# Kernel tuning notes

Measured on AMD Instinct MI355X. Metric: run time of the kernel, lower is better.

The kernel has to match this reference:

```python
import jax, jax.numpy as jnp
import numpy as np

DIM = 1280
NUM_HEADS = 16
HEAD_DIM = DIM // NUM_HEADS  # 80
SEQ = 3072


def rotate_half(x):
    half = x.shape[-1] // 2
    return jnp.concatenate([-x[..., half:], x[..., :half]], axis=-1)


def apply_rotary_pos_emb_vision(t, freqs):
    # t: [seq, heads, head_dim]; freqs: [seq, head_dim//2]
    emb = jnp.concatenate([freqs, freqs], axis=-1)  # [seq, head_dim]
    cos = jnp.cos(emb)[:, None, :]
    sin = jnp.sin(emb)[:, None, :]
    return t * cos + rotate_half(t) * sin


def setup_inputs() -> dict:
    key = jax.random.key(0)
    k1, k2, k3, k4, k5 = jax.random.split(key, 5)
    hidden_states = jax.random.normal(k1, (SEQ, DIM), dtype=jnp.float32)
    rotary_pos_emb = jax.random.uniform(k2, (SEQ, HEAD_DIM // 2), dtype=jnp.float32) * 10.0
    cu_seqlens = jnp.arange(5, dtype=jnp.int32) * (SEQ // 4)  # [0,768,1536,2304,3072]
    s = 1.0 / np.sqrt(DIM)
    qkv_w = jax.random.normal(k3, (3 * DIM, DIM), dtype=jnp.float32) * s
    qkv_b = jnp.zeros((3 * DIM,), dtype=jnp.float32)
    proj_w = jax.random.normal(k4, (DIM, DIM), dtype=jnp.float32) * s
    proj_b = jnp.zeros((DIM,), dtype=jnp.float32)
    return {
        "hidden_states": hidden_states,
        "rotary_pos_emb": rotary_pos_emb,
        "cu_seqlens": cu_seqlens,
        "qkv_w": qkv_w,
        "qkv_b": qkv_b,
        "proj_w": proj_w,
        "proj_b": proj_b,
    }


def reference(hidden_states, rotary_pos_emb, cu_seqlens, qkv_w, qkv_b, proj_w, proj_b):
    seq = hidden_states.shape[0]
    qkv = hidden_states @ qkv_w.T + qkv_b  # [seq, 3*dim]
    qkv = qkv.reshape(seq, 3, NUM_HEADS, HEAD_DIM)
    q, k, v = qkv[:, 0], qkv[:, 1], qkv[:, 2]  # each [seq, heads, head_dim]

    q = apply_rotary_pos_emb_vision(q, rotary_pos_emb)
    k = apply_rotary_pos_emb_vision(k, rotary_pos_emb)

    # block-diagonal mask from cu_seqlens: tokens attend only within own segment
    pos = jnp.arange(seq)
    seg = jnp.searchsorted(cu_seqlens[1:], pos, side="right")  # segment id per token
    mask = seg[:, None] == seg[None, :]  # [seq, seq] bool

    # [heads, seq, head_dim]
    qh = q.transpose(1, 0, 2)
    kh = k.transpose(1, 0, 2)
    vh = v.transpose(1, 0, 2)

    scale = 1.0 / np.sqrt(HEAD_DIM)
    scores = jnp.einsum("hqd,hkd->hqk", qh, kh) * scale
    scores = jnp.where(mask[None], scores, jnp.finfo(scores.dtype).min)
    attn = jax.nn.softmax(scores, axis=-1)
    out = jnp.einsum("hqk,hkd->hqd", attn, vh)  # [heads, seq, head_dim]

    out = out.transpose(1, 0, 2).reshape(seq, DIM)
    return out @ proj_w.T + proj_b
```

## Files before the change

### kernel.cpp

```cpp
#include <hip/hip_runtime.h>
#include <cstdint>
#include <cstddef>

#define SEQ 3072
#define DIM 1280
#define NH 16
#define HD 80

typedef __attribute__((ext_vector_type(8))) short s16x8;
typedef __attribute__((ext_vector_type(4))) float f32x4;
typedef unsigned short u16;
typedef unsigned int u32;
typedef unsigned long long u64;

__device__ __forceinline__ u16 f2bf(float f) {
  u32 u = __builtin_bit_cast(u32, f);
  u32 r = (u + 0x7FFFu + ((u >> 16) & 1u)) >> 16;
  return (u16)r;
}
__device__ __forceinline__ float bf2f(u16 b) {
  u32 u = ((u32)b) << 16;
  return __builtin_bit_cast(float, u);
}
__device__ __forceinline__ u32 cvtpk_bf16(float lo, float hi) {
  u32 r;
  asm("v_cvt_pk_bf16_f32 %0, %1, %2" : "=v"(r) : "v"(lo), "v"(hi));
  return r;
}
__device__ __forceinline__ void gload16(const u16* g, u16* lds) {
  __builtin_amdgcn_global_load_lds((const __attribute__((address_space(1))) void*)g,
                                   (__attribute__((address_space(3))) void*)lds,
                                   16, 0, 0);
}

#define N4_A (SEQ*DIM/4)
#define N4_B (3*DIM*DIM/4)
#define N4_C (DIM*DIM/4)
__global__ void cvt_kernel(const float* __restrict__ sa, u16* __restrict__ da,
                           const float* __restrict__ sb, u16* __restrict__ db,
                           const float* __restrict__ sc, u16* __restrict__ dc) {
  int i = blockIdx.x * blockDim.x + threadIdx.x;
  const float* s; u16* d; int j;
  if (i < N4_A)            { s = sa; d = da; j = i; }
  else if (i < N4_A+N4_B)  { s = sb; d = db; j = i - N4_A; }
  else if (i < N4_A+N4_B+N4_C) { s = sc; d = dc; j = i - N4_A - N4_B; }
  else return;
  float4 v = ((const float4*)s)[j];
  ushort4 o;
  o.x = f2bf(v.x); o.y = f2bf(v.y); o.z = f2bf(v.z); o.w = f2bf(v.w);
  ((ushort4*)d)[j] = o;
}

template<int MODE>
__global__ __launch_bounds__(256)
void gemm_kernel(const u16* __restrict__ A, const u16* __restrict__ B,
                 const float* __restrict__ bias,
                 u16* __restrict__ qws, u16* __restrict__ kws, u16* __restrict__ vT,
                 float* __restrict__ fout,
                 int M, int N, int K)
{
  constexpr int BM = 128, BN = 128, BK = 32;
  __shared__ __align__(16) u16 As[2][BM*BK];
  __shared__ __align__(16) u16 Bs[2][BN*BK];
  const int m0 = blockIdx.y * BM, n0 = blockIdx.x * BN;
  const int tid = threadIdx.x;
  const int lane = tid & 63, wave = tid >> 6;
  const int wr = wave >> 1, wc = wave & 1;
  const int lr = lane & 15, lg = lane >> 4;

  const int c0 = tid, c1 = 256 + tid;
  const int r0 = c0 >> 2, cc0 = c0 & 3;
  const int r1 = c1 >> 2, cc1 = c1 & 3;
  const int wb0 = (tid & ~63), wb1 = 256 + (tid & ~63);

  f32x4 acc[4][4];
  #pragma unroll
  for (int i = 0; i < 4; ++i)
    #pragma unroll
    for (int j = 0; j < 4; ++j) acc[i][j] = (f32x4)0.0f;

  const int NT = K / BK;

  gload16(A + (size_t)(m0 + r0)*K + cc0*8, &As[0][0] + wb0*8);
  gload16(B + (size_t)(n0 + r0)*K + cc0*8, &Bs[0][0] + wb0*8);
  gload16(A + (size_t)(m0 + r1)*K + cc1*8, &As[0][0] + wb1*8);
  gload16(B + (size_t)(n0 + r1)*K + cc1*8, &Bs[0][0] + wb1*8);
  __syncthreads();

  int cur = 0;
  for (int t = 0; t < NT; ++t) {
    if (t + 1 < NT) {
      const int k0 = (t + 1) * BK;
      const int nxt = cur ^ 1;
      gload16(A + (size_t)(m0 + r0)*K + k0 + cc0*8, &As[nxt][0] + wb0*8);
      gload16(B + (size_t)(n0 + r0)*K + k0 + cc0*8, &Bs[nxt][0] + wb0*8);
      gload16(A + (size_t)(m0 + r1)*K + k0 + cc1*8, &As[nxt][0] + wb1*8);
      gload16(B + (size_t)(n0 + r1)*K + k0 + cc1*8, &Bs[nxt][0] + wb1*8);
    }
    s16x8 af[4], bf[4];
    #pragma unroll
    for (int i = 0; i < 4; ++i) {
      af[i] = *(const s16x8*)&As[cur][(wr*64 + i*16 + lr)*BK + lg*8];
      bf[i] = *(const s16x8*)&Bs[cur][(wc*64 + i*16 + lr)*BK + lg*8];
    }
    #pragma unroll
    for (int mi = 0; mi < 4; ++mi)
      #pragma unroll
      for (int ni = 0; ni < 4; ++ni)
        acc[mi][ni] = __builtin_amdgcn_mfma_f32_16x16x32_bf16(af[mi], bf[ni], acc[mi][ni], 0, 0, 0);
    __syncthreads();
    cur ^= 1;
  }

  #pragma unroll
  for (int ni = 0; ni < 4; ++ni) {
    const int n = n0 + wc*64 + ni*16 + lr;
    const float bv = bias[n];
    if constexpr (MODE == 0) {
      const int which = n / DIM;
      const int hd = n - which*DIM;
      const int h = hd / HD;
      const int d = hd - h*HD;
      #pragma unroll
      for (int mi = 0; mi < 4; ++mi) {
        const int mb = m0 + wr*64 + mi*16 + lg*4;
        #pragma unroll
        for (int j = 0; j < 4; ++j) {
          const u16 b = f2bf(acc[mi][ni][j] + bv);
          const int m = mb + j;
          if (which == 0)      qws[((size_t)h*SEQ + m)*HD + d] = b;
          else if (which == 1) kws[((size_t)h*SEQ + m)*HD + d] = b;
          else                 vT [((size_t)h*HD + d)*SEQ + m] = b;
        }
      }
    } else {
      #pragma unroll
      for (int mi = 0; mi < 4; ++mi) {
        const int mb = m0 + wr*64 + mi*16 + lg*4;
        #pragma unroll
        for (int j = 0; j < 4; ++j)
          fout[(size_t)(mb + j)*N + n] = acc[mi][ni][j] + bv;
      }
    }
  }
}

__global__ void rope_tab_kernel(const float* __restrict__ freqs, float2* __restrict__ tab, int n) {
  int i = blockIdx.x*blockDim.x + threadIdx.x;
  if (i >= n) return;
  float f = freqs[i];
  tab[i] = make_float2(cosf(f), sinf(f));
}

__global__ void rope_apply_kernel(u16* __restrict__ q, u16* __restrict__ k,
                                  const float2* __restrict__ tab) {
  int idx = blockIdx.x*blockDim.x + threadIdx.x;
  if (idx >= NH*SEQ*5) return;
  const int c = idx % 5;
  const int s = (idx / 5) % SEQ;
  const int h = idx / (5*SEQ);
  const int d0 = c*8;
  const float2* tp = tab + s*(HD/2) + d0;
  float cs[8], sn[8];
  #pragma unroll
  for (int j = 0; j < 8; ++j) { float2 f = tp[j]; cs[j] = f.x; sn[j] = f.y; }
  const size_t base = ((size_t)h*SEQ + s)*HD;
  {
    s16x8 x = *(const s16x8*)(q + base + d0);
    s16x8 y = *(const s16x8*)(q + base + (HD/2) + d0);
    s16x8 nx, ny;
    #pragma unroll
    for (int j = 0; j < 8; ++j) {
      float xv = bf2f((u16)x[j]), yv = bf2f((u16)y[j]);
      nx[j] = (short)f2bf(xv*cs[j] - yv*sn[j]);
      ny[j] = (short)f2bf(yv*cs[j] + xv*sn[j]);
    }
    *(s16x8*)(q + base + d0) = nx;
    *(s16x8*)(q + base + (HD/2) + d0) = ny;
  }
  {
    s16x8 x = *(const s16x8*)(k + base + d0);
    s16x8 y = *(const s16x8*)(k + base + (HD/2) + d0);
    s16x8 nx, ny;
    #pragma unroll
    for (int j = 0; j < 8; ++j) {
      float xv = bf2f((u16)x[j]), yv = bf2f((u16)y[j]);
      nx[j] = (short)f2bf(xv*cs[j] - yv*sn[j]);
      ny[j] = (short)f2bf(yv*cs[j] + xv*sn[j]);
    }
    *(s16x8*)(k + base + d0) = nx;
    *(s16x8*)(k + base + (HD/2) + d0) = ny;
  }
}


struct AttnState {
  float m_run[2];
  float lp[2];
  f32x4 oacc[2][5];
};

__device__ __forceinline__ void load_kv(const u16* __restrict__ kbase,
                                        const u16* __restrict__ vbase,
                                        int lr, int lg, int kc,
                                        s16x8 (&KF)[2][3], s16x8 (&VF)[5]) {
  int kcl = kc; if (kcl > SEQ-32) kcl = SEQ-32;
  #pragma unroll
  for (int kt = 0; kt < 2; ++kt)
    #pragma unroll
    for (int s = 0; s < 3; ++s) {
      const int d0 = s*32 + lg*8;
      if (d0 < HD) KF[kt][s] = *(const s16x8*)(kbase + (size_t)(kcl + kt*16 + lr)*HD + d0);
      else         KF[kt][s] = (s16x8)(short)0;
    }
  #pragma unroll
  for (int dt = 0; dt < 5; ++dt)
    VF[dt] = *(const s16x8*)(vbase + (size_t)(dt*16 + lr)*SEQ + kcl + lg*8);
}

__device__ __forceinline__ void compute_chunk(int kc, const s16x8 (&KF)[2][3], const s16x8 (&VF)[5],
                                              const s16x8 (&qf)[2][3], AttnState& st,
                                              u16 (&P_lds)[2][16][32],
                                              int lr, int lg, int swz,
                                              int rs0, int re0, int rs1, int re1) {
  const float NEG = -__builtin_inff();
  const float DTH = 8.0f;
  const float kscale = 0.11180339887498949f * 1.44269504088896341f;

  f32x4 sacc[2][2];
  #pragma unroll
  for (int qs = 0; qs < 2; ++qs)
    #pragma unroll
    for (int kt = 0; kt < 2; ++kt) sacc[qs][kt] = (f32x4)0.0f;
  #pragma unroll
  for (int kt = 0; kt < 2; ++kt)
    #pragma unroll
    for (int s = 0; s < 3; ++s) {
      sacc[0][kt] = __builtin_amdgcn_mfma_f32_16x16x32_bf16(KF[kt][s], qf[0][s], sacc[0][kt], 0, 0, 0);
      sacc[1][kt] = __builtin_amdgcn_mfma_f32_16x16x32_bf16(KF[kt][s], qf[1][s], sacc[1][kt], 0, 0, 0);
    }

  float sv[2][8];
  #pragma unroll
  for (int qs = 0; qs < 2; ++qs)
    #pragma unroll
    for (int kt = 0; kt < 2; ++kt)
      #pragma unroll
      for (int j = 0; j < 4; ++j)
        sv[qs][kt*4+j] = sacc[qs][kt][j] * kscale;

  const bool full = __all((kc >= rs0) && (kc+32 <= re0) && (kc >= rs1) && (kc+32 <= re1));
  if (!full) {
    #pragma unroll
    for (int qs = 0; qs < 2; ++qs) {
      const int rsq = qs ? rs1 : rs0, req = qs ? re1 : re0;
      #pragma unroll
      for (int kt = 0; kt < 2; ++kt)
        #pragma unroll
        for (int j = 0; j < 4; ++j) {
          const int key = kc + kt*16 + lg*4 + j;
          if (key < rsq || key >= req) sv[qs][kt*4+j] = NEG;
        }
    }
  }

  float pc[2];
  #pragma unroll
  for (int qs = 0; qs < 2; ++qs) {
    float c = sv[qs][0];
    #pragma unroll
    for (int i = 1; i < 8; ++i) c = fmaxf(c, sv[qs][i]);
    pc[qs] = c;
  }

  const bool nore = __all((pc[0] - st.m_run[0] <= DTH) && (pc[1] - st.m_run[1] <= DTH));
  u32 pk[2][4];
  if (nore) {
    #pragma unroll
    for (int qs = 0; qs < 2; ++qs) {
      const float m = st.m_run[qs];
      float ps = 0.0f;
      #pragma unroll
      for (int i2 = 0; i2 < 4; ++i2) {
        float pa = __builtin_amdgcn_exp2f(sv[qs][2*i2]   - m);
        float pb = __builtin_amdgcn_exp2f(sv[qs][2*i2+1] - m);
        ps += pa + pb;
        pk[qs][i2] = cvtpk_bf16(pa, pb);
      }
      st.lp[qs] += ps;
    }
  } else {
    #pragma unroll
    for (int qs = 0; qs < 2; ++qs) {
      float c = pc[qs];
      c = fmaxf(c, __shfl_xor(c, 16, 64));
      c = fmaxf(c, __shfl_xor(c, 32, 64));
      const float mn = fmaxf(st.m_run[qs], c);
      const float fs = (mn == st.m_run[qs]) ? 1.0f : __builtin_amdgcn_exp2f(st.m_run[qs] - mn);
      float ps = 0.0f;
      #pragma unroll
      for (int i2 = 0; i2 < 4; ++i2) {
        float a0 = sv[qs][2*i2], a1 = sv[qs][2*i2+1];
        float pa = (a0 == NEG) ? 0.0f : __builtin_amdgcn_exp2f(a0 - mn);
        float pb = (a1 == NEG) ? 0.0f : __builtin_amdgcn_exp2f(a1 - mn);
        ps += pa + pb;
        pk[qs][i2] = cvtpk_bf16(pa, pb);
      }
      st.lp[qs] = st.lp[qs] * fs + ps;
      st.m_run[qs] = mn;
      float fr[4];
      #pragma unroll
      for (int j = 0; j < 4; ++j)
        fr[j] = __builtin_bit_cast(float,
                  __builtin_amdgcn_ds_bpermute((lg*4 + j)*4, __builtin_bit_cast(int, fs)));
      #pragma unroll
      for (int dt = 0; dt < 5; ++dt)
        #pragma unroll
        for (int j = 0; j < 4; ++j) st.oacc[qs][dt][j] *= fr[j];
    }
  }

  #pragma unroll
  for (int qs = 0; qs < 2; ++qs) {
    u64 w0 = (u64)pk[qs][0] | ((u64)pk[qs][1] << 32);
    u64 w1 = (u64)pk[qs][2] | ((u64)pk[qs][3] << 32);
    u64* P64 = (u64*)&P_lds[qs][0][0];
    P64[lr*8 + ( lg      ^ (swz<<1))] = w0;
    P64[lr*8 + ((4 + lg) ^ (swz<<1))] = w1;
  }
  s16x8 pa0 = *(const s16x8*)&P_lds[0][lr][(lg ^ swz) * 8];
  s16x8 pa1 = *(const s16x8*)&P_lds[1][lr][(lg ^ swz) * 8];

  #pragma unroll
  for (int dt = 0; dt < 5; ++dt) {
    st.oacc[0][dt] = __builtin_amdgcn_mfma_f32_16x16x32_bf16(pa0, VF[dt], st.oacc[0][dt], 0, 0, 0);
    st.oacc[1][dt] = __builtin_amdgcn_mfma_f32_16x16x32_bf16(pa1, VF[dt], st.oacc[1][dt], 0, 0, 0);
  }
}

__global__ __launch_bounds__(64)
void attn_kernel(const u16* __restrict__ qws, const u16* __restrict__ kws,
                 const u16* __restrict__ vT, const int* __restrict__ cu, int ncu,
                 u16* __restrict__ ows )
{
  __shared__ __align__(16) u16 P_lds[2][16][32];
  const int h = blockIdx.x & 15;
  const int t = blockIdx.x >> 4;
  const int lane = threadIdx.x;
  const int lr = lane & 15, lg = lane >> 4;
  const int q0 = t*32;
  const float NEG = -__builtin_inff();

  int rs0 = cu[0], re0 = cu[1], rs1 = cu[0], re1 = cu[1];
  int ts = cu[0], te = cu[1];
  {
    const int qa = q0 + lr, qb = q0 + 16 + lr;
    for (int i = 1; i < ncu-1; ++i) {
      int lo = cu[i], hi = cu[i+1];
      if (qa    >= lo) { rs0 = lo; re0 = hi; }
      if (qb    >= lo) { rs1 = lo; re1 = hi; }
      if (q0    >= lo) { ts = lo; }
      if (q0+31 >= lo) { te = hi; }
    }
  }

  const u16* kbase = kws + (size_t)h*SEQ*HD;
  const u16* vbase = vT  + (size_t)h*HD*SEQ;

  s16x8 qf[2][3];
  #pragma unroll
  for (int qs = 0; qs < 2; ++qs)
    #pragma unroll
    for (int s = 0; s < 3; ++s) {
      int d0 = s*32 + lg*8;
      if (d0 < HD) qf[qs][s] = *(const s16x8*)(qws + ((size_t)h*SEQ + q0 + qs*16 + lr)*HD + d0);
      else         qf[qs][s] = (s16x8)(short)0;
    }

  AttnState st;
  st.m_run[0] = NEG; st.m_run[1] = NEG;
  st.lp[0] = 0.0f;   st.lp[1] = 0.0f;
  #pragma unroll
  for (int qs = 0; qs < 2; ++qs)
    #pragma unroll
    for (int dt = 0; dt < 5; ++dt) st.oacc[qs][dt] = (f32x4)0.0f;

  const int swz = (lr >> 1) & 3;

  const int kc0 = ts & ~31;
  const int nch = (te - kc0 + 31) >> 5;

  s16x8 kfA[2][3], vfA[5], kfB[2][3], vfB[5];
  load_kv(kbase, vbase, lr, lg, kc0, kfA, vfA);

  int kc = kc0, i = 0;
  for (; i + 2 <= nch; i += 2) {
    load_kv(kbase, vbase, lr, lg, kc+32, kfB, vfB);
    compute_chunk(kc, kfA, vfA, qf, st, P_lds, lr, lg, swz, rs0, re0, rs1, re1);
    load_kv(kbase, vbase, lr, lg, kc+64, kfA, vfA);
    compute_chunk(kc+32, kfB, vfB, qf, st, P_lds, lr, lg, swz, rs0, re0, rs1, re1);
    kc += 64;
  }
  if (i < nch)
    compute_chunk(kc, kfA, vfA, qf, st, P_lds, lr, lg, swz, rs0, re0, rs1, re1);

  #pragma unroll
  for (int qs = 0; qs < 2; ++qs) {
    float l = st.lp[qs];
    l += __shfl_xor(l, 16, 64);
    l += __shfl_xor(l, 32, 64);
    float linv[4];
    #pragma unroll
    for (int j = 0; j < 4; ++j) {
      float lv = __builtin_bit_cast(float,
                   __builtin_amdgcn_ds_bpermute((lg*4 + j)*4, __builtin_bit_cast(int, l)));
      linv[j] = 1.0f / lv;
    }
    #pragma unroll
    for (int dt = 0; dt < 5; ++dt)
      #pragma unroll
      for (int j = 0; j < 4; ++j) {
        float v = st.oacc[qs][dt][j] * linv[j];
        ows[(size_t)(q0 + qs*16 + lg*4 + j)*DIM + h*HD + dt*16 + lr] = f2bf(v);
      }
  }
}

extern "C" void kernel_launch(void* const* d_in, const int* in_sizes, int n_in,
                              void* d_out, int out_size, void* d_ws, size_t ws_size,
                              hipStream_t stream) {
  const float* hidden = (const float*)d_in[0];
  const float* rope   = (const float*)d_in[1];
  const int*   cu     = (const int*)d_in[2];
  const float* qkv_w  = (const float*)d_in[3];
  const float* qkv_b  = (const float*)d_in[4];
  const float* proj_w = (const float*)d_in[5];
  const float* proj_b = (const float*)d_in[6];
  float* out = (float*)d_out;
  const int ncu = in_sizes[2];

  char* ws = (char*)d_ws;
  u16* Abf = (u16*)ws; ws += (size_t)SEQ*DIM*2;
  u16* Wq  = (u16*)ws; ws += (size_t)3*DIM*DIM*2;
  u16* Wp  = (u16*)ws; ws += (size_t)DIM*DIM*2;
  u16* qws = (u16*)ws; ws += (size_t)NH*SEQ*HD*2;
  u16* kws = (u16*)ws; ws += (size_t)NH*SEQ*HD*2;
  u16* vTw = (u16*)ws; ws += (size_t)NH*SEQ*HD*2;
  u16* ows = (u16*)ws; ws += (size_t)SEQ*DIM*2;

  cvt_kernel<<<(N4_A+N4_B+N4_C+255)/256, 256, 0, stream>>>(hidden, Abf, qkv_w, Wq, proj_w, Wp);

  gemm_kernel<0><<<dim3(3*DIM/128, SEQ/128), 256, 0, stream>>>(
      Abf, Wq, qkv_b, qws, kws, vTw, nullptr, SEQ, 3*DIM, DIM);

  float2* tab = (float2*)Abf;
  rope_tab_kernel<<<(SEQ*(HD/2) + 255)/256, 256, 0, stream>>>(rope, tab, SEQ*(HD/2));
  rope_apply_kernel<<<(NH*SEQ*5 + 255)/256, 256, 0, stream>>>(qws, kws, tab);

  attn_kernel<<<NH*(SEQ/32), 64, 0, stream>>>(qws, kws, vTw, cu, ncu, ows);

  gemm_kernel<1><<<dim3(DIM/128, SEQ/128), 256, 0, stream>>>(
      ows, Wp, proj_b, nullptr, nullptr, nullptr, out, SEQ, DIM, DIM);
}
```

Measured before the change: 156.4 us.

## Triple-buffer GEMM loads with vmcnt waits and shrink attention blocks to 16 queries

The GEMM now prefetches two K-tiles ahead and uses explicit vmcnt/lgkmcnt waits with raw barriers in place of __syncthreads, so global loads can overlap more MFMA work. The attention kernel processes 16 queries per wavefront instead of 32, doubling the grid to raise occupancy and parallelism. It also adds a third K/V register buffer for a deeper software pipeline. The trade-off is that each K/V chunk is loaded for half as many queries, doubling K/V load traffic, and the hand-written waitcnt logic depends on how the compiler orders loads.

```diff
diff --git a/kernel.cpp b/kernel.cpp
--- a/kernel.cpp
+++ b/kernel.cpp
@@ -73,6 +73,14 @@
   const int r1 = c1 >> 2, cc1 = c1 & 3;
   const int wb0 = (tid & ~63), wb1 = 256 + (tid & ~63);
 
+  auto stage = [&](int t, int buf) {
+    const int k0 = t * BK;
+    gload16(A + (size_t)(m0 + r0)*K + k0 + cc0*8, &As[buf][0] + wb0*8);
+    gload16(B + (size_t)(n0 + r0)*K + k0 + cc0*8, &Bs[buf][0] + wb0*8);
+    gload16(A + (size_t)(m0 + r1)*K + k0 + cc1*8, &As[buf][0] + wb1*8);
+    gload16(B + (size_t)(n0 + r1)*K + k0 + cc1*8, &Bs[buf][0] + wb1*8);
+  };
+
   f32x4 acc[4][4];
   #pragma unroll
   for (int i = 0; i < 4; ++i)
@@ -81,22 +89,16 @@
 
   const int NT = K / BK;
 
-  gload16(A + (size_t)(m0 + r0)*K + cc0*8, &As[0][0] + wb0*8);
-  gload16(B + (size_t)(n0 + r0)*K + cc0*8, &Bs[0][0] + wb0*8);
-  gload16(A + (size_t)(m0 + r1)*K + cc1*8, &As[0][0] + wb1*8);
-  gload16(B + (size_t)(n0 + r1)*K + cc1*8, &Bs[0][0] + wb1*8);
-  __syncthreads();
+  stage(0, 0);
+  stage(1, 1);
 
   int cur = 0;
   for (int t = 0; t < NT; ++t) {
-    if (t + 1 < NT) {
-      const int k0 = (t + 1) * BK;
-      const int nxt = cur ^ 1;
-      gload16(A + (size_t)(m0 + r0)*K + k0 + cc0*8, &As[nxt][0] + wb0*8);
-      gload16(B + (size_t)(n0 + r0)*K + k0 + cc0*8, &Bs[nxt][0] + wb0*8);
-      gload16(A + (size_t)(m0 + r1)*K + k0 + cc1*8, &As[nxt][0] + wb1*8);
-      gload16(B + (size_t)(n0 + r1)*K + k0 + cc1*8, &Bs[nxt][0] + wb1*8);
-    }
+    if (t == NT - 1) asm volatile("s_waitcnt vmcnt(0)" ::: "memory");
+    else             asm volatile("s_waitcnt vmcnt(4)" ::: "memory");
+    __builtin_amdgcn_s_barrier();
+    __builtin_amdgcn_sched_barrier(0);
+
     s16x8 af[4], bf[4];
     #pragma unroll
     for (int i = 0; i < 4; ++i) {
@@ -108,7 +110,12 @@
       #pragma unroll
       for (int ni = 0; ni < 4; ++ni)
         acc[mi][ni] = __builtin_amdgcn_mfma_f32_16x16x32_bf16(af[mi], bf[ni], acc[mi][ni], 0, 0, 0);
-    __syncthreads();
+
+    asm volatile("s_waitcnt lgkmcnt(0)" ::: "memory");
+    __builtin_amdgcn_sched_barrier(0);
+    __builtin_amdgcn_s_barrier();
+
+    if (t + 2 < NT) stage(t + 2, cur);
     cur ^= 1;
   }
 
@@ -195,9 +202,9 @@
 
 
 struct AttnState {
-  float m_run[2];
-  float lp[2];
-  f32x4 oacc[2][5];
+  float m_run;
+  float lp;
+  f32x4 oacc[5];
 };
 
 __device__ __forceinline__ void load_kv(const u16* __restrict__ kbase,
@@ -219,123 +226,98 @@
 }
 
 __device__ __forceinline__ void compute_chunk(int kc, const s16x8 (&KF)[2][3], const s16x8 (&VF)[5],
-                                              const s16x8 (&qf)[2][3], AttnState& st,
-                                              u16 (&P_lds)[2][16][32],
+                                              const s16x8 (&qf)[3], AttnState& st,
+                                              u16 (&P_lds)[16][32],
                                               int lr, int lg, int swz,
-                                              int rs0, int re0, int rs1, int re1) {
+                                              int rs0, int re0) {
   const float NEG = -__builtin_inff();
   const float DTH = 8.0f;
   const float kscale = 0.11180339887498949f * 1.44269504088896341f;
 
-  f32x4 sacc[2][2];
-  #pragma unroll
-  for (int qs = 0; qs < 2; ++qs)
-    #pragma unroll
-    for (int kt = 0; kt < 2; ++kt) sacc[qs][kt] = (f32x4)0.0f;
+  f32x4 sacc[2];
+  #pragma unroll
+  for (int kt = 0; kt < 2; ++kt) sacc[kt] = (f32x4)0.0f;
   #pragma unroll
   for (int kt = 0; kt < 2; ++kt)
     #pragma unroll
-    for (int s = 0; s < 3; ++s) {
-      sacc[0][kt] = __builtin_amdgcn_mfma_f32_16x16x32_bf16(KF[kt][s], qf[0][s], sacc[0][kt], 0, 0, 0);
-      sacc[1][kt] = __builtin_amdgcn_mfma_f32_16x16x32_bf16(KF[kt][s], qf[1][s], sacc[1][kt], 0, 0, 0);
-    }
-
-  float sv[2][8];
-  #pragma unroll
-  for (int qs = 0; qs < 2; ++qs)
+    for (int s = 0; s < 3; ++s)
+      sacc[kt] = __builtin_amdgcn_mfma_f32_16x16x32_bf16(KF[kt][s], qf[s], sacc[kt], 0, 0, 0);
+
+  float sv[8];
+  #pragma unroll
+  for (int kt = 0; kt < 2; ++kt)
+    #pragma unroll
+    for (int j = 0; j < 4; ++j)
+      sv[kt*4+j] = sacc[kt][j] * kscale;
+
+  const bool full = __all((kc >= rs0) && (kc+32 <= re0));
+  if (!full) {
     #pragma unroll
     for (int kt = 0; kt < 2; ++kt)
       #pragma unroll
-      for (int j = 0; j < 4; ++j)
-        sv[qs][kt*4+j] = sacc[qs][kt][j] * kscale;
-
-  const bool full = __all((kc >= rs0) && (kc+32 <= re0) && (kc >= rs1) && (kc+32 <= re1));
-  if (!full) {
-    #pragma unroll
-    for (int qs = 0; qs < 2; ++qs) {
-      const int rsq = qs ? rs1 : rs0, req = qs ? re1 : re0;
-      #pragma unroll
-      for (int kt = 0; kt < 2; ++kt)
-        #pragma unroll
-        for (int j = 0; j < 4; ++j) {
-          const int key = kc + kt*16 + lg*4 + j;
-          if (key < rsq || key >= req) sv[qs][kt*4+j] = NEG;
-        }
-    }
-  }
-
-  float pc[2];
-  #pragma unroll
-  for (int qs = 0; qs < 2; ++qs) {
-    float c = sv[qs][0];
-    #pragma unroll
-    for (int i = 1; i < 8; ++i) c = fmaxf(c, sv[qs][i]);
-    pc[qs] = c;
-  }
-
-  const bool nore = __all((pc[0] - st.m_run[0] <= DTH) && (pc[1] - st.m_run[1] <= DTH));
-  u32 pk[2][4];
+      for (int j = 0; j < 4; ++j) {
+        const int key = kc + kt*16 + lg*4 + j;
+        if (key < rs0 || key >= re0) sv[kt*4+j] = NEG;
+      }
+  }
+
+  float pc = sv[0];
+  #pragma unroll
+  for (int i = 1; i < 8; ++i) pc = fmaxf(pc, sv[i]);
+
+  const bool nore = __all(pc - st.m_run <= DTH);
+  u32 pk[4];
   if (nore) {
-    #pragma unroll
-    for (int qs = 0; qs < 2; ++qs) {
-      const float m = st.m_run[qs];
-      float ps = 0.0f;
-      #pragma unroll
-      for (int i2 = 0; i2 < 4; ++i2) {
-        float pa = __builtin_amdgcn_exp2f(sv[qs][2*i2]   - m);
-        float pb = __builtin_amdgcn_exp2f(sv[qs][2*i2+1] - m);
-        ps += pa + pb;
-        pk[qs][i2] = cvtpk_bf16(pa, pb);
-      }
-      st.lp[qs] += ps;
-    }
+    const float m = st.m_run;
+    float ps = 0.0f;
+    #pragma unroll
+    for (int i2 = 0; i2 < 4; ++i2) {
+      float pa = __builtin_amdgcn_exp2f(sv[2*i2]   - m);
+      float pb = __builtin_amdgcn_exp2f(sv[2*i2+1] - m);
+      ps += pa + pb;
+      pk[i2] = cvtpk_bf16(pa, pb);
+    }
+    st.lp += ps;
   } else {
-    #pragma unroll
-    for (int qs = 0; qs < 2; ++qs) {
-      float c = pc[qs];
-      c = fmaxf(c, __shfl_xor(c, 16, 64));
-      c = fmaxf(c, __shfl_xor(c, 32, 64));
-      const float mn = fmaxf(st.m_run[qs], c);
-      const float fs = (mn == st.m_run[qs]) ? 1.0f : __builtin_amdgcn_exp2f(st.m_run[qs] - mn);
-      float ps = 0.0f;
-      #pragma unroll
-      for (int i2 = 0; i2 < 4; ++i2) {
-        float a0 = sv[qs][2*i2], a1 = sv[qs][2*i2+1];
-        float pa = (a0 == NEG) ? 0.0f : __builtin_amdgcn_exp2f(a0 - mn);
-        float pb = (a1 == NEG) ? 0.0f : __builtin_amdgcn_exp2f(a1 - mn);
-        ps += pa + pb;
-        pk[qs][i2] = cvtpk_bf16(pa, pb);
-      }
-      st.lp[qs] = st.lp[qs] * fs + ps;
-      st.m_run[qs] = mn;
-      float fr[4];
-      #pragma unroll
-      for (int j = 0; j < 4; ++j)
-        fr[j] = __builtin_bit_cast(float,
-                  __builtin_amdgcn_ds_bpermute((lg*4 + j)*4, __builtin_bit_cast(int, fs)));
-      #pragma unroll
-      for (int dt = 0; dt < 5; ++dt)
-        #pragma unroll
-        for (int j = 0; j < 4; ++j) st.oacc[qs][dt][j] *= fr[j];
-    }
-  }
-
-  #pragma unroll
-  for (int qs = 0; qs < 2; ++qs) {
-    u64 w0 = (u64)pk[qs][0] | ((u64)pk[qs][1] << 32);
-    u64 w1 = (u64)pk[qs][2] | ((u64)pk[qs][3] << 32);
-    u64* P64 = (u64*)&P_lds[qs][0][0];
+    float c = pc;
+    c = fmaxf(c, __shfl_xor(c, 16, 64));
+    c = fmaxf(c, __shfl_xor(c, 32, 64));
+    const float mn = fmaxf(st.m_run, c);
+    const float fs = (mn == st.m_run) ? 1.0f : __builtin_amdgcn_exp2f(st.m_run - mn);
+    float ps = 0.0f;
+    #pragma unroll
+    for (int i2 = 0; i2 < 4; ++i2) {
+      float a0 = sv[2*i2], a1 = sv[2*i2+1];
+      float pa = (a0 == NEG) ? 0.0f : __builtin_amdgcn_exp2f(a0 - mn);
+      float pb = (a1 == NEG) ? 0.0f : __builtin_amdgcn_exp2f(a1 - mn);
+      ps += pa + pb;
+      pk[i2] = cvtpk_bf16(pa, pb);
+    }
+    st.lp = st.lp * fs + ps;
+    st.m_run = mn;
+    float fr[4];
+    #pragma unroll
+    for (int j = 0; j < 4; ++j)
+      fr[j] = __builtin_bit_cast(float,
+                __builtin_amdgcn_ds_bpermute((lg*4 + j)*4, __builtin_bit_cast(int, fs)));
+    #pragma unroll
+    for (int dt = 0; dt < 5; ++dt)
+      #pragma unroll
+      for (int j = 0; j < 4; ++j) st.oacc[dt][j] *= fr[j];
+  }
+
+  {
+    u64 w0 = (u64)pk[0] | ((u64)pk[1] << 32);
+    u64 w1 = (u64)pk[2] | ((u64)pk[3] << 32);
+    u64* P64 = (u64*)&P_lds[0][0];
     P64[lr*8 + ( lg      ^ (swz<<1))] = w0;
     P64[lr*8 + ((4 + lg) ^ (swz<<1))] = w1;
   }
-  s16x8 pa0 = *(const s16x8*)&P_lds[0][lr][(lg ^ swz) * 8];
-  s16x8 pa1 = *(const s16x8*)&P_lds[1][lr][(lg ^ swz) * 8];
-
-  #pragma unroll
-  for (int dt = 0; dt < 5; ++dt) {
-    st.oacc[0][dt] = __builtin_amdgcn_mfma_f32_16x16x32_bf16(pa0, VF[dt], st.oacc[0][dt], 0, 0, 0);
-    st.oacc[1][dt] = __builtin_amdgcn_mfma_f32_16x16x32_bf16(pa1, VF[dt], st.oacc[1][dt], 0, 0, 0);
-  }
+  s16x8 pa = *(const s16x8*)&P_lds[lr][(lg ^ swz) * 8];
+
+  #pragma unroll
+  for (int dt = 0; dt < 5; ++dt)
+    st.oacc[dt] = __builtin_amdgcn_mfma_f32_16x16x32_bf16(pa, VF[dt], st.oacc[dt], 0, 0, 0);
 }
 
 __global__ __launch_bounds__(64)
@@ -343,70 +325,68 @@
                  const u16* __restrict__ vT, const int* __restrict__ cu, int ncu,
                  u16* __restrict__ ows )
 {
-  __shared__ __align__(16) u16 P_lds[2][16][32];
+  __shared__ __align__(16) u16 P_lds[16][32];
   const int h = blockIdx.x & 15;
   const int t = blockIdx.x >> 4;
   const int lane = threadIdx.x;
   const int lr = lane & 15, lg = lane >> 4;
-  const int q0 = t*32;
+  const int q0 = t*16;
   const float NEG = -__builtin_inff();
 
-  int rs0 = cu[0], re0 = cu[1], rs1 = cu[0], re1 = cu[1];
+  int rs0 = cu[0], re0 = cu[1];
   int ts = cu[0], te = cu[1];
   {
-    const int qa = q0 + lr, qb = q0 + 16 + lr;
+    const int qa = q0 + lr;
     for (int i = 1; i < ncu-1; ++i) {
       int lo = cu[i], hi = cu[i+1];
       if (qa    >= lo) { rs0 = lo; re0 = hi; }
-      if (qb    >= lo) { rs1 = lo; re1 = hi; }
       if (q0    >= lo) { ts = lo; }
-      if (q0+31 >= lo) { te = hi; }
+      if (q0+15 >= lo) { te = hi; }
     }
   }
 
   const u16* kbase = kws + (size_t)h*SEQ*HD;
   const u16* vbase = vT  + (size_t)h*HD*SEQ;
 
-  s16x8 qf[2][3];
-  #pragma unroll
-  for (int qs = 0; qs < 2; ++qs)
-    #pragma unroll
-    for (int s = 0; s < 3; ++s) {
-      int d0 = s*32 + lg*8;
-      if (d0 < HD) qf[qs][s] = *(const s16x8*)(qws + ((size_t)h*SEQ + q0 + qs*16 + lr)*HD + d0);
-      else         qf[qs][s] = (s16x8)(short)0;
-    }
+  s16x8 qf[3];
+  #pragma unroll
+  for (int s = 0; s < 3; ++s) {
+    int d0 = s*32 + lg*8;
+    if (d0 < HD) qf[s] = *(const s16x8*)(qws + ((size_t)h*SEQ + q0 + lr)*HD + d0);
+    else         qf[s] = (s16x8)(short)0;
+  }
 
   AttnState st;
-  st.m_run[0] = NEG; st.m_run[1] = NEG;
-  st.lp[0] = 0.0f;   st.lp[1] = 0.0f;
-  #pragma unroll
-  for (int qs = 0; qs < 2; ++qs)
-    #pragma unroll
-    for (int dt = 0; dt < 5; ++dt) st.oacc[qs][dt] = (f32x4)0.0f;
+  st.m_run = NEG;
+  st.lp = 0.0f;
+  #pragma unroll
+  for (int dt = 0; dt < 5; ++dt) st.oacc[dt] = (f32x4)0.0f;
 
   const int swz = (lr >> 1) & 3;
 
   const int kc0 = ts & ~31;
   const int nch = (te - kc0 + 31) >> 5;
 
-  s16x8 kfA[2][3], vfA[5], kfB[2][3], vfB[5];
-  load_kv(kbase, vbase, lr, lg, kc0, kfA, vfA);
+  s16x8 kfA[2][3], vfA[5], kfB[2][3], vfB[5], kfC[2][3], vfC[5];
+  load_kv(kbase, vbase, lr, lg, kc0,      kfA, vfA);
+  load_kv(kbase, vbase, lr, lg, kc0 + 32, kfB, vfB);
 
   int kc = kc0, i = 0;
-  for (; i + 2 <= nch; i += 2) {
-    load_kv(kbase, vbase, lr, lg, kc+32, kfB, vfB);
-    compute_chunk(kc, kfA, vfA, qf, st, P_lds, lr, lg, swz, rs0, re0, rs1, re1);
-    load_kv(kbase, vbase, lr, lg, kc+64, kfA, vfA);
-    compute_chunk(kc+32, kfB, vfB, qf, st, P_lds, lr, lg, swz, rs0, re0, rs1, re1);
-    kc += 64;
-  }
-  if (i < nch)
-    compute_chunk(kc, kfA, vfA, qf, st, P_lds, lr, lg, swz, rs0, re0, rs1, re1);
-
-  #pragma unroll
-  for (int qs = 0; qs < 2; ++qs) {
-    float l = st.lp[qs];
+  for (; i + 3 <= nch; i += 3) {
+    load_kv(kbase, vbase, lr, lg, kc+64,  kfC, vfC);
+    compute_chunk(kc,    kfA, vfA, qf, st, P_lds, lr, lg, swz, rs0, re0);
+    load_kv(kbase, vbase, lr, lg, kc+96,  kfA, vfA);
+    compute_chunk(kc+32, kfB, vfB, qf, st, P_lds, lr, lg, swz, rs0, re0);
+    load_kv(kbase, vbase, lr, lg, kc+128, kfB, vfB);
+    compute_chunk(kc+64, kfC, vfC, qf, st, P_lds, lr, lg, swz, rs0, re0);
+    kc += 96;
+  }
+  const int rem = nch - i;
+  if (rem >= 1) compute_chunk(kc,    kfA, vfA, qf, st, P_lds, lr, lg, swz, rs0, re0);
+  if (rem == 2) compute_chunk(kc+32, kfB, vfB, qf, st, P_lds, lr, lg, swz, rs0, re0);
+
+  {
+    float l = st.lp;
     l += __shfl_xor(l, 16, 64);
     l += __shfl_xor(l, 32, 64);
     float linv[4];
@@ -420,8 +400,8 @@
     for (int dt = 0; dt < 5; ++dt)
       #pragma unroll
       for (int j = 0; j < 4; ++j) {
-        float v = st.oacc[qs][dt][j] * linv[j];
-        ows[(size_t)(q0 + qs*16 + lg*4 + j)*DIM + h*HD + dt*16 + lr] = f2bf(v);
+        float v = st.oacc[dt][j] * linv[j];
+        ows[(size_t)(q0 + lg*4 + j)*DIM + h*HD + dt*16 + lr] = f2bf(v);
       }
   }
 }
@@ -457,7 +437,7 @@
   rope_tab_kernel<<<(SEQ*(HD/2) + 255)/256, 256, 0, stream>>>(rope, tab, SEQ*(HD/2));
   rope_apply_kernel<<<(NH*SEQ*5 + 255)/256, 256, 0, stream>>>(qws, kws, tab);
 
-  attn_kernel<<<NH*(SEQ/32), 64, 0, stream>>>(qws, kws, vTw, cu, ncu, ows);
+  attn_kernel<<<NH*(SEQ/16), 64, 0, stream>>>(qws, kws, vTw, cu, ncu, ows);
 
   gemm_kernel<1><<<dim3(DIM/128, SEQ/128), 256, 0, stream>>>(
       ows, Wp, proj_b, nullptr, nullptr, nullptr, out, SEQ, DIM, DIM);
```

Measured after the change: 168.5 us. 7.7% more time.

## Share K/V tiles across two waves via double-buffered LDS staging in attention

Applied to the files above, without the earlier changes.

The attention kernel now launches 128-thread blocks covering 64 query rows. K and V chunks of 64 keys are loaded cooperatively into double-buffered shared memory with direct global-to-LDS loads, and both waves read their MFMA operands from there. Each K/V tile is fetched from global memory once per two waves instead of once per wave, and the key chunk grows from 32 to 64. The costs are a __syncthreads per chunk, more LDS per block, and more registers for the larger score tile, which may lower occupancy. Segment bounds are now computed over the 64-row block, so waves near segment edges can scan more masked keys.

```diff
diff --git a/kernel.cpp b/kernel.cpp
--- a/kernel.cpp
+++ b/kernel.cpp
@@ -6,6 +6,8 @@
 #define DIM 1280
 #define NH 16
 #define HD 80
+#define QB 64
+#define KB 64
 
 typedef __attribute__((ext_vector_type(8))) short s16x8;
 typedef __attribute__((ext_vector_type(4))) float f32x4;
@@ -193,179 +195,63 @@
   }
 }
 
-
-struct AttnState {
-  float m_run[2];
-  float lp[2];
-  f32x4 oacc[2][5];
-};
-
-__device__ __forceinline__ void load_kv(const u16* __restrict__ kbase,
-                                        const u16* __restrict__ vbase,
-                                        int lr, int lg, int kc,
-                                        s16x8 (&KF)[2][3], s16x8 (&VF)[5]) {
-  int kcl = kc; if (kcl > SEQ-32) kcl = SEQ-32;
-  #pragma unroll
-  for (int kt = 0; kt < 2; ++kt)
-    #pragma unroll
-    for (int s = 0; s < 3; ++s) {
-      const int d0 = s*32 + lg*8;
-      if (d0 < HD) KF[kt][s] = *(const s16x8*)(kbase + (size_t)(kcl + kt*16 + lr)*HD + d0);
-      else         KF[kt][s] = (s16x8)(short)0;
-    }
-  #pragma unroll
-  for (int dt = 0; dt < 5; ++dt)
-    VF[dt] = *(const s16x8*)(vbase + (size_t)(dt*16 + lr)*SEQ + kcl + lg*8);
-}
-
-__device__ __forceinline__ void compute_chunk(int kc, const s16x8 (&KF)[2][3], const s16x8 (&VF)[5],
-                                              const s16x8 (&qf)[2][3], AttnState& st,
-                                              u16 (&P_lds)[2][16][32],
-                                              int lr, int lg, int swz,
-                                              int rs0, int re0, int rs1, int re1) {
-  const float NEG = -__builtin_inff();
-  const float DTH = 8.0f;
-  const float kscale = 0.11180339887498949f * 1.44269504088896341f;
-
-  f32x4 sacc[2][2];
-  #pragma unroll
-  for (int qs = 0; qs < 2; ++qs)
-    #pragma unroll
-    for (int kt = 0; kt < 2; ++kt) sacc[qs][kt] = (f32x4)0.0f;
-  #pragma unroll
-  for (int kt = 0; kt < 2; ++kt)
-    #pragma unroll
-    for (int s = 0; s < 3; ++s) {
-      sacc[0][kt] = __builtin_amdgcn_mfma_f32_16x16x32_bf16(KF[kt][s], qf[0][s], sacc[0][kt], 0, 0, 0);
-      sacc[1][kt] = __builtin_amdgcn_mfma_f32_16x16x32_bf16(KF[kt][s], qf[1][s], sacc[1][kt], 0, 0, 0);
-    }
-
-  float sv[2][8];
-  #pragma unroll
-  for (int qs = 0; qs < 2; ++qs)
-    #pragma unroll
-    for (int kt = 0; kt < 2; ++kt)
-      #pragma unroll
-      for (int j = 0; j < 4; ++j)
-        sv[qs][kt*4+j] = sacc[qs][kt][j] * kscale;
-
-  const bool full = __all((kc >= rs0) && (kc+32 <= re0) && (kc >= rs1) && (kc+32 <= re1));
-  if (!full) {
-    #pragma unroll
-    for (int qs = 0; qs < 2; ++qs) {
-      const int rsq = qs ? rs1 : rs0, req = qs ? re1 : re0;
-      #pragma unroll
-      for (int kt = 0; kt < 2; ++kt)
-        #pragma unroll
-        for (int j = 0; j < 4; ++j) {
-          const int key = kc + kt*16 + lg*4 + j;
-          if (key < rsq || key >= req) sv[qs][kt*4+j] = NEG;
-        }
-    }
-  }
-
-  float pc[2];
-  #pragma unroll
-  for (int qs = 0; qs < 2; ++qs) {
-    float c = sv[qs][0];
-    #pragma unroll
-    for (int i = 1; i < 8; ++i) c = fmaxf(c, sv[qs][i]);
-    pc[qs] = c;
-  }
-
-  const bool nore = __all((pc[0] - st.m_run[0] <= DTH) && (pc[1] - st.m_run[1] <= DTH));
-  u32 pk[2][4];
-  if (nore) {
-    #pragma unroll
-    for (int qs = 0; qs < 2; ++qs) {
-      const float m = st.m_run[qs];
-      float ps = 0.0f;
-      #pragma unroll
-      for (int i2 = 0; i2 < 4; ++i2) {
-        float pa = __builtin_amdgcn_exp2f(sv[qs][2*i2]   - m);
-        float pb = __builtin_amdgcn_exp2f(sv[qs][2*i2+1] - m);
-        ps += pa + pb;
-        pk[qs][i2] = cvtpk_bf16(pa, pb);
-      }
-      st.lp[qs] += ps;
-    }
-  } else {
-    #pragma unroll
-    for (int qs = 0; qs < 2; ++qs) {
-      float c = pc[qs];
-      c = fmaxf(c, __shfl_xor(c, 16, 64));
-      c = fmaxf(c, __shfl_xor(c, 32, 64));
-      const float mn = fmaxf(st.m_run[qs], c);
-      const float fs = (mn == st.m_run[qs]) ? 1.0f : __builtin_amdgcn_exp2f(st.m_run[qs] - mn);
-      float ps = 0.0f;
-      #pragma unroll
-      for (int i2 = 0; i2 < 4; ++i2) {
-        float a0 = sv[qs][2*i2], a1 = sv[qs][2*i2+1];
-        float pa = (a0 == NEG) ? 0.0f : __builtin_amdgcn_exp2f(a0 - mn);
-        float pb = (a1 == NEG) ? 0.0f : __builtin_amdgcn_exp2f(a1 - mn);
-        ps += pa + pb;
-        pk[qs][i2] = cvtpk_bf16(pa, pb);
-      }
-      st.lp[qs] = st.lp[qs] * fs + ps;
-      st.m_run[qs] = mn;
-      float fr[4];
-      #pragma unroll
-      for (int j = 0; j < 4; ++j)
-        fr[j] = __builtin_bit_cast(float,
-                  __builtin_amdgcn_ds_bpermute((lg*4 + j)*4, __builtin_bit_cast(int, fs)));
-      #pragma unroll
-      for (int dt = 0; dt < 5; ++dt)
-        #pragma unroll
-        for (int j = 0; j < 4; ++j) st.oacc[qs][dt][j] *= fr[j];
-    }
-  }
-
-  #pragma unroll
-  for (int qs = 0; qs < 2; ++qs) {
-    u64 w0 = (u64)pk[qs][0] | ((u64)pk[qs][1] << 32);
-    u64 w1 = (u64)pk[qs][2] | ((u64)pk[qs][3] << 32);
-    u64* P64 = (u64*)&P_lds[qs][0][0];
-    P64[lr*8 + ( lg      ^ (swz<<1))] = w0;
-    P64[lr*8 + ((4 + lg) ^ (swz<<1))] = w1;
-  }
-  s16x8 pa0 = *(const s16x8*)&P_lds[0][lr][(lg ^ swz) * 8];
-  s16x8 pa1 = *(const s16x8*)&P_lds[1][lr][(lg ^ swz) * 8];
-
-  #pragma unroll
-  for (int dt = 0; dt < 5; ++dt) {
-    st.oacc[0][dt] = __builtin_amdgcn_mfma_f32_16x16x32_bf16(pa0, VF[dt], st.oacc[0][dt], 0, 0, 0);
-    st.oacc[1][dt] = __builtin_amdgcn_mfma_f32_16x16x32_bf16(pa1, VF[dt], st.oacc[1][dt], 0, 0, 0);
-  }
-}
-
-__global__ __launch_bounds__(64)
+__global__ __launch_bounds__(128)
 void attn_kernel(const u16* __restrict__ qws, const u16* __restrict__ kws,
                  const u16* __restrict__ vT, const int* __restrict__ cu, int ncu,
                  u16* __restrict__ ows )
 {
-  __shared__ __align__(16) u16 P_lds[2][16][32];
+  __shared__ __align__(16) u16 Ks[2][KB*HD];
+  __shared__ __align__(16) u16 Vs[2][HD*KB];
+  __shared__ __align__(16) u16 P_lds[2][2][16*72];
   const int h = blockIdx.x & 15;
   const int t = blockIdx.x >> 4;
-  const int lane = threadIdx.x;
+  const int tid = threadIdx.x;
+  const int w = tid >> 6;
+  const int lane = tid & 63;
   const int lr = lane & 15, lg = lane >> 4;
-  const int q0 = t*32;
+  const int q0 = t*QB + w*32;
   const float NEG = -__builtin_inff();
+  const float DTH = 8.0f;
+  const float kscale = 0.11180339887498949f * 1.44269504088896341f;
 
   int rs0 = cu[0], re0 = cu[1], rs1 = cu[0], re1 = cu[1];
   int ts = cu[0], te = cu[1];
   {
     const int qa = q0 + lr, qb = q0 + 16 + lr;
+    const int qblk = t*QB;
     for (int i = 1; i < ncu-1; ++i) {
       int lo = cu[i], hi = cu[i+1];
-      if (qa    >= lo) { rs0 = lo; re0 = hi; }
-      if (qb    >= lo) { rs1 = lo; re1 = hi; }
-      if (q0    >= lo) { ts = lo; }
-      if (q0+31 >= lo) { te = hi; }
+      if (qa        >= lo) { rs0 = lo; re0 = hi; }
+      if (qb        >= lo) { rs1 = lo; re1 = hi; }
+      if (qblk      >= lo) { ts = lo; }
+      if (qblk+QB-1 >= lo) { te = hi; }
     }
   }
 
   const u16* kbase = kws + (size_t)h*SEQ*HD;
   const u16* vbase = vT  + (size_t)h*HD*SEQ;
+
+  int rK[5], cK[5], dV[5], cV[5];
+  #pragma unroll
+  for (int i = 0; i < 5; ++i) {
+    const int c = i*128 + tid;
+    rK[i] = c / 10; cK[i] = c % 10;
+    dV[i] = c >> 3; cV[i] = (c & 7) ^ (dV[i] & 7);
+  }
+  const int wub = (tid & ~63);
+
+  auto stage = [&](int kc, int buf) {
+    #pragma unroll
+    for (int i = 0; i < 5; ++i) {
+      int rr = kc + rK[i]; if (rr > SEQ-1) rr = SEQ-1;
+      gload16(kbase + (size_t)rr*HD + cK[i]*8, &Ks[buf][0] + (i*128 + wub)*8);
+    }
+    #pragma unroll
+    for (int i = 0; i < 5; ++i) {
+      int colc = kc + cV[i]*8; if (colc > SEQ-8) colc = SEQ-8;
+      gload16(vbase + (size_t)dV[i]*SEQ + colc, &Vs[buf][0] + (i*128 + wub)*8);
+    }
+  };
 
   s16x8 qf[2][3];
   #pragma unroll
@@ -377,36 +263,150 @@
       else         qf[qs][s] = (s16x8)(short)0;
     }
 
-  AttnState st;
-  st.m_run[0] = NEG; st.m_run[1] = NEG;
-  st.lp[0] = 0.0f;   st.lp[1] = 0.0f;
+  float m_run[2] = {NEG, NEG};
+  float lp[2]    = {0.0f, 0.0f};
+  f32x4 oacc[2][5];
   #pragma unroll
   for (int qs = 0; qs < 2; ++qs)
     #pragma unroll
-    for (int dt = 0; dt < 5; ++dt) st.oacc[qs][dt] = (f32x4)0.0f;
+    for (int dt = 0; dt < 5; ++dt) oacc[qs][dt] = (f32x4)0.0f;
 
   const int swz = (lr >> 1) & 3;
-
-  const int kc0 = ts & ~31;
-  const int nch = (te - kc0 + 31) >> 5;
-
-  s16x8 kfA[2][3], vfA[5], kfB[2][3], vfB[5];
-  load_kv(kbase, vbase, lr, lg, kc0, kfA, vfA);
-
-  int kc = kc0, i = 0;
-  for (; i + 2 <= nch; i += 2) {
-    load_kv(kbase, vbase, lr, lg, kc+32, kfB, vfB);
-    compute_chunk(kc, kfA, vfA, qf, st, P_lds, lr, lg, swz, rs0, re0, rs1, re1);
-    load_kv(kbase, vbase, lr, lg, kc+64, kfA, vfA);
-    compute_chunk(kc+32, kfB, vfB, qf, st, P_lds, lr, lg, swz, rs0, re0, rs1, re1);
-    kc += 64;
-  }
-  if (i < nch)
-    compute_chunk(kc, kfA, vfA, qf, st, P_lds, lr, lg, swz, rs0, re0, rs1, re1);
+  const int kc0 = ts & ~(KB-1);
+
+  stage(kc0, 0);
+  __syncthreads();
+
+  int cur = 0;
+  for (int kc = kc0; kc < te; kc += KB) {
+    if (kc + KB < te) stage(kc + KB, cur ^ 1);
+
+    f32x4 sacc[2][4];
+    #pragma unroll
+    for (int qs = 0; qs < 2; ++qs)
+      #pragma unroll
+      for (int kt = 0; kt < 4; ++kt) sacc[qs][kt] = (f32x4)0.0f;
+    #pragma unroll
+    for (int kt = 0; kt < 4; ++kt)
+      #pragma unroll
+      for (int s = 0; s < 3; ++s) {
+        s16x8 kf = *(const s16x8*)&Ks[cur][(kt*16 + lr)*HD + s*32 + lg*8];
+        sacc[0][kt] = __builtin_amdgcn_mfma_f32_16x16x32_bf16(kf, qf[0][s], sacc[0][kt], 0, 0, 0);
+        sacc[1][kt] = __builtin_amdgcn_mfma_f32_16x16x32_bf16(kf, qf[1][s], sacc[1][kt], 0, 0, 0);
+      }
+
+    float sv[2][16];
+    #pragma unroll
+    for (int qs = 0; qs < 2; ++qs)
+      #pragma unroll
+      for (int kt = 0; kt < 4; ++kt)
+        #pragma unroll
+        for (int j = 0; j < 4; ++j)
+          sv[qs][kt*4+j] = sacc[qs][kt][j] * kscale;
+
+    const bool full = __all((kc >= rs0) && (kc+KB <= re0) && (kc >= rs1) && (kc+KB <= re1));
+    if (!full) {
+      #pragma unroll
+      for (int qs = 0; qs < 2; ++qs) {
+        const int rsq = qs ? rs1 : rs0, req = qs ? re1 : re0;
+        #pragma unroll
+        for (int kt = 0; kt < 4; ++kt)
+          #pragma unroll
+          for (int j = 0; j < 4; ++j) {
+            const int key = kc + kt*16 + lg*4 + j;
+            if (key < rsq || key >= req) sv[qs][kt*4+j] = NEG;
+          }
+      }
+    }
+
+    float pc[2];
+    #pragma unroll
+    for (int qs = 0; qs < 2; ++qs) {
+      float c = sv[qs][0];
+      #pragma unroll
+      for (int i = 1; i < 16; ++i) c = fmaxf(c, sv[qs][i]);
+      pc[qs] = c;
+    }
+    const bool nore = __all((pc[0] - m_run[0] <= DTH) && (pc[1] - m_run[1] <= DTH));
+    u32 pk[2][8];
+    if (nore) {
+      #pragma unroll
+      for (int qs = 0; qs < 2; ++qs) {
+        const float m = m_run[qs];
+        float ps = 0.0f;
+        #pragma unroll
+        for (int i2 = 0; i2 < 8; ++i2) {
+          float pa = __builtin_amdgcn_exp2f(sv[qs][2*i2]   - m);
+          float pb = __builtin_amdgcn_exp2f(sv[qs][2*i2+1] - m);
+          ps += pa + pb;
+          pk[qs][i2] = cvtpk_bf16(pa, pb);
+        }
+        lp[qs] += ps;
+      }
+    } else {
+      #pragma unroll
+      for (int qs = 0; qs < 2; ++qs) {
+        float c = pc[qs];
+        c = fmaxf(c, __shfl_xor(c, 16, 64));
+        c = fmaxf(c, __shfl_xor(c, 32, 64));
+        const float mn = fmaxf(m_run[qs], c);
+        const float fs = (mn == m_run[qs]) ? 1.0f : __builtin_amdgcn_exp2f(m_run[qs] - mn);
+        float ps = 0.0f;
+        #pragma unroll
+        for (int i2 = 0; i2 < 8; ++i2) {
+          float a0 = sv[qs][2*i2], a1 = sv[qs][2*i2+1];
+          float pa = (a0 == NEG) ? 0.0f : __builtin_amdgcn_exp2f(a0 - mn);
+          float pb = (a1 == NEG) ? 0.0f : __builtin_amdgcn_exp2f(a1 - mn);
+          ps += pa + pb;
+          pk[qs][i2] = cvtpk_bf16(pa, pb);
+        }
+        lp[qs] = lp[qs] * fs + ps;
+        m_run[qs] = mn;
+        float fr[4];
+        #pragma unroll
+        for (int j = 0; j < 4; ++j)
+          fr[j] = __builtin_bit_cast(float,
+                    __builtin_amdgcn_ds_bpermute((lg*4 + j)*4, __builtin_bit_cast(int, fs)));
+        #pragma unroll
+        for (int dt = 0; dt < 5; ++dt)
+          #pragma unroll
+          for (int j = 0; j < 4; ++j) oacc[qs][dt][j] *= fr[j];
+      }
+    }
+
+    s16x8 pa[2][2];
+    #pragma unroll
+    for (int qs = 0; qs < 2; ++qs) {
+      u64* P64 = (u64*)&P_lds[w][qs][0];
+      const int e0 =  lg      ^ (swz<<1);
+      const int e1 = (4 + lg) ^ (swz<<1);
+      P64[lr*18 +     e0] = (u64)pk[qs][0] | ((u64)pk[qs][1] << 32);
+      P64[lr*18 +     e1] = (u64)pk[qs][2] | ((u64)pk[qs][3] << 32);
+      P64[lr*18 + 8 + e0] = (u64)pk[qs][4] | ((u64)pk[qs][5] << 32);
+      P64[lr*18 + 8 + e1] = (u64)pk[qs][6] | ((u64)pk[qs][7] << 32);
+    }
+    #pragma unroll
+    for (int qs = 0; qs < 2; ++qs) {
+      pa[qs][0] = *(const s16x8*)&P_lds[w][qs][lr*72 +      (lg ^ swz)*8];
+      pa[qs][1] = *(const s16x8*)&P_lds[w][qs][lr*72 + 32 + (lg ^ swz)*8];
+    }
+
+    #pragma unroll
+    for (int dt = 0; dt < 5; ++dt)
+      #pragma unroll
+      for (int kg = 0; kg < 2; ++kg) {
+        s16x8 vf = *(const s16x8*)&Vs[cur][(dt*16 + lr)*KB + (((kg*4 + lg) ^ (lr & 7))*8)];
+        oacc[0][dt] = __builtin_amdgcn_mfma_f32_16x16x32_bf16(pa[0][kg], vf, oacc[0][dt], 0, 0, 0);
+        oacc[1][dt] = __builtin_amdgcn_mfma_f32_16x16x32_bf16(pa[1][kg], vf, oacc[1][dt], 0, 0, 0);
+      }
+
+    __syncthreads();
+    cur ^= 1;
+  }
 
   #pragma unroll
   for (int qs = 0; qs < 2; ++qs) {
-    float l = st.lp[qs];
+    float l = lp[qs];
     l += __shfl_xor(l, 16, 64);
     l += __shfl_xor(l, 32, 64);
     float linv[4];
@@ -420,7 +420,7 @@
     for (int dt = 0; dt < 5; ++dt)
       #pragma unroll
       for (int j = 0; j < 4; ++j) {
-        float v = st.oacc[qs][dt][j] * linv[j];
+        float v = oacc[qs][dt][j] * linv[j];
         ows[(size_t)(q0 + qs*16 + lg*4 + j)*DIM + h*HD + dt*16 + lr] = f2bf(v);
       }
   }
@@ -457,7 +457,7 @@
   rope_tab_kernel<<<(SEQ*(HD/2) + 255)/256, 256, 0, stream>>>(rope, tab, SEQ*(HD/2));
   rope_apply_kernel<<<(NH*SEQ*5 + 255)/256, 256, 0, stream>>>(qws, kws, tab);
 
-  attn_kernel<<<NH*(SEQ/32), 64, 0, stream>>>(qws, kws, vTw, cu, ncu, ows);
+  attn_kernel<<<NH*(SEQ/QB), 128, 0, stream>>>(qws, kws, vTw, cu, ncu, ows);
 
   gemm_kernel<1><<<dim3(DIM/128, SEQ/128), 256, 0, stream>>>(
       ows, Wp, proj_b, nullptr, nullptr, nullptr, out, SEQ, DIM, DIM);
```

Result: slower. 162.8 us (+4.1%).
